# Kernel tuning notes

Hardware: AMD Instinct MI355X
Metric: run time of the kernel (lower is better)

The kernel has to match this reference:

```python
import jax, jax.numpy as jnp
import numpy as np

TAU = 0.05


def setup_inputs() -> dict:
    key = jax.random.key(0)
    ks = jax.random.split(key, 4)
    N, D, F, E = 8192, 1024, 4096, 8
    h = jax.random.normal(ks[0], (N, D), dtype=jnp.float32)
    Wr = jax.random.normal(ks[1], (D, E), dtype=jnp.float32) * (1.0 / np.sqrt(D))
    br = jnp.zeros((E,), dtype=jnp.float32)
    W1 = jax.random.normal(ks[2], (E, D, F), dtype=jnp.float32) * (1.0 / np.sqrt(D))
    b1 = jnp.zeros((E, F), dtype=jnp.float32)
    W2 = jax.random.normal(ks[3], (E, F, D), dtype=jnp.float32) * (1.0 / np.sqrt(F))
    b2 = jnp.zeros((E, D), dtype=jnp.float32)
    return {"h": h, "Wr": Wr, "br": br, "W1": W1, "b1": b1, "W2": W2, "b2": b2}


def reference(h, Wr, br, W1, b1, W2, b2):
    # Router: linear + softmax over experts -> [N, E]
    weights = jax.nn.softmax(h @ Wr + br, axis=-1)
    # Threshold mask (weights > tau); masked_weights = weights * mask
    masked_w = jnp.where(weights > TAU, weights, 0.0)  # [N, E]
    # Experts: 2-layer MLP per expert, computed batched over the expert axis.
    # hid: [N, E, F]
    hid = jax.nn.gelu(jnp.einsum('nd,edf->nef', h, W1) + b1)
    # expert outputs: [N, E, D]
    out_e = jnp.einsum('nef,efd->ned', hid, W2) + b2
    # Weighted combine; zero masked weights annihilate inactive experts,
    # matching the conditional sum (and the zeros_like fallback when none active).
    return jnp.einsum('ne,ned->nd', masked_w, out_e)
```

## Files before the change

### kernel.cpp

```cpp
#include <hip/hip_runtime.h>
#include <hip/hip_bf16.h>
#include <cstdint>
#include <cstddef>

typedef __attribute__((ext_vector_type(8))) __bf16 bf16x8;
typedef __attribute__((ext_vector_type(4))) float f32x4;
typedef __attribute__((ext_vector_type(4))) unsigned short us4;

#define GLOAD_LDS16(g, l)                                                        \
    __builtin_amdgcn_global_load_lds(                                            \
        (const __attribute__((address_space(1))) void*)(g),                      \
        (__attribute__((address_space(3))) void*)(l), 16, 0, 0)

static __device__ __forceinline__ unsigned short f2bf(float x) {
    unsigned int u = __builtin_bit_cast(unsigned int, x);
    return (unsigned short)((u + 0x7FFFu + ((u >> 16) & 1u)) >> 16);
}

static __device__ __forceinline__ float gelu_fast(float x) {
    const float p = x * x;
    const float u = x * fmaf(0.0713548162726f, p, 1.59576912161f);
    const float t = __expf(-u);
    return x * __builtin_amdgcn_rcpf(1.0f + t);
}

__global__ __launch_bounds__(256) void moe_router_kernel(
    const float* __restrict__ h, const float* __restrict__ Wr,
    const float* __restrict__ br, unsigned short* __restrict__ hbf,
    float* __restrict__ mw)
{
    const int lane = threadIdx.x & 63, wave = threadIdx.x >> 6;
    const int n = blockIdx.x * 4 + wave;
    const float* hr = h + (size_t)n * 1024;
    const int base = lane * 16;

    float xs[16];
#pragma unroll
    for (int q = 0; q < 4; ++q) {
        f32x4 v = *(const f32x4*)(hr + base + q * 4);
        xs[q * 4 + 0] = v[0]; xs[q * 4 + 1] = v[1];
        xs[q * 4 + 2] = v[2]; xs[q * 4 + 3] = v[3];
    }
    float acc[8] = {0.f, 0.f, 0.f, 0.f, 0.f, 0.f, 0.f, 0.f};
#pragma unroll
    for (int j = 0; j < 16; ++j) {
        const float x = xs[j];
        const f32x4 w0 = *(const f32x4*)(Wr + (size_t)(base + j) * 8);
        const f32x4 w1 = *(const f32x4*)(Wr + (size_t)(base + j) * 8 + 4);
        acc[0] += x * w0[0]; acc[1] += x * w0[1]; acc[2] += x * w0[2]; acc[3] += x * w0[3];
        acc[4] += x * w1[0]; acc[5] += x * w1[1]; acc[6] += x * w1[2]; acc[7] += x * w1[3];
    }
#pragma unroll
    for (int q = 0; q < 4; ++q) {
        us4 o;
        o[0] = f2bf(xs[q * 4 + 0]); o[1] = f2bf(xs[q * 4 + 1]);
        o[2] = f2bf(xs[q * 4 + 2]); o[3] = f2bf(xs[q * 4 + 3]);
        *(us4*)(hbf + (size_t)n * 1024 + base + q * 4) = o;
    }
#pragma unroll
    for (int m = 32; m >= 1; m >>= 1)
#pragma unroll
        for (int e = 0; e < 8; ++e) acc[e] += __shfl_xor(acc[e], m, 64);

    if (lane == 0) {
        float l[8]; float mx = -1e30f;
#pragma unroll
        for (int e = 0; e < 8; ++e) { l[e] = acc[e] + br[e]; mx = fmaxf(mx, l[e]); }
        float s = 0.f;
#pragma unroll
        for (int e = 0; e < 8; ++e) { l[e] = __expf(l[e] - mx); s += l[e]; }
        const float inv = 1.0f / s;
#pragma unroll
        for (int e = 0; e < 8; ++e) {
            const float w = l[e] * inv;
            mw[(size_t)n * 8 + e] = (w > 0.05f) ? w : 0.0f;
        }
    }
}

__global__ __launch_bounds__(256) void moe_tcvt_kernel(
    const float* __restrict__ in, unsigned short* __restrict__ out,
    int ls, size_t in_es, int os, size_t out_es)
{
    __shared__ unsigned short t[32][33];
    const int e = blockIdx.z;
    const int r = threadIdx.x >> 3, c = (threadIdx.x & 7) * 4;
    const float* I = in + (size_t)e * in_es + (size_t)(blockIdx.x * 32 + r) * ls + blockIdx.y * 32 + c;
    f32x4 v = *(const f32x4*)I;
    t[r][c + 0] = f2bf(v[0]); t[r][c + 1] = f2bf(v[1]);
    t[r][c + 2] = f2bf(v[2]); t[r][c + 3] = f2bf(v[3]);
    __syncthreads();
    unsigned short* O = out + (size_t)e * out_es + (size_t)(blockIdx.y * 32 + r) * os + blockIdx.x * 32 + c;
    us4 o;
    o[0] = t[c + 0][r]; o[1] = t[c + 1][r]; o[2] = t[c + 2][r]; o[3] = t[c + 3][r];
    *(us4*)O = o;
}

#define MFMA_QUAD(MB, NB, AF, BQ)                                              \
  _Pragma("unroll") for (int mi_ = 0; mi_ < 4; ++mi_)                          \
  _Pragma("unroll") for (int ni_ = 0; ni_ < 2; ++ni_) {                        \
      acc[(MB)+mi_][(NB)+ni_] = __builtin_amdgcn_mfma_f32_16x16x32_bf16(       \
          BQ[ni_][1], AF[mi_][1], __builtin_amdgcn_mfma_f32_16x16x32_bf16(     \
          BQ[ni_][0], AF[mi_][0], acc[(MB)+mi_][(NB)+ni_], 0, 0, 0), 0, 0, 0); \
  }

#define BARX()   __builtin_amdgcn_s_barrier()
#define SBX()    __builtin_amdgcn_sched_barrier(0)
#define LGKM(N)  asm volatile("s_waitcnt lgkmcnt(" #N ")" ::: "memory")
#define VMC(N)   asm volatile("s_waitcnt vmcnt(" #N ")" ::: "memory")
#define PRIO1()  __builtin_amdgcn_s_setprio(1)
#define PRIO0()  __builtin_amdgcn_s_setprio(0)

template <int MODE>
__global__ __launch_bounds__(512) void moe_gemm8p(
    const unsigned short* __restrict__ A, int ldga,
    const unsigned short* __restrict__ Bbase, size_t estride, int ldb,
    const float* __restrict__ b1, const float* __restrict__ mw,
    unsigned short* __restrict__ Cg, int ldc,
    float* __restrict__ part,
    int logFc, int f0glob, int kspan, int init)
{
    __shared__ unsigned short sh[65536];
    char* sm = (char*)sh;
    const int XA = 0, XB = 32768, YA = 65536, YB = 98304;

    const int tid = threadIdx.x, lane = tid & 63, wv = tid >> 6;
    const int wr = wv >> 2, wc = wv & 3;

    int bx, by;
    if constexpr (MODE == 0) {
        const int gy = gridDim.y;
        const int orig = blockIdx.x + blockIdx.y * 32;
        const int c8 = orig & 7, j = orig >> 3;
        bx = c8 * 4 + j / gy; by = j % gy;
    } else {
        const int orig = blockIdx.x + blockIdx.y * 32;
        const int c8 = orig & 7, j = orig >> 3;
        bx = c8 * 4 + (j >> 2); by = j & 3;
    }
    const int m0 = bx * 256;
    const int n0 = by * 256;

    const int z = (MODE == 1) ? blockIdx.z : 0;
    const int klo = z * kspan;
    float* Cacc = (MODE == 1) ? part + (size_t)z * (8192 * 1024) : nullptr;

    int e0 = 0, fb = 0;
    const unsigned short* gB0 = nullptr;
    const int rl0 = tid >> 3;
    const int gs8 = ((tid & 7) ^ (rl0 & 7)) * 8;
    if constexpr (MODE == 0) {
        e0 = n0 >> logFc; fb = n0 - (e0 << logFc);
        gB0 = Bbase + (size_t)e0 * estride + (size_t)(fb + rl0) * ldb + gs8;
    }
    const unsigned short* gA0 = A + (size_t)(m0 + rl0) * ldga + gs8;
    const int dstw = wv * 1024;

    auto stageA = [&](int reg, int kk, int q) {
        GLOAD_LDS16(gA0 + kk + (size_t)(q * 64) * ldga,
                    sm + reg + (q >> 1) * 16384 + (q & 1) * 8192 + dstw);
    };
    auto stageB = [&](int reg, int kk, int q) {
        const unsigned short* gb;
        if constexpr (MODE == 0) {
            gb = gB0 + kk;
        } else {
            const int e = kk >> logFc, kc = kk - (e << logFc);
            gb = Bbase + (size_t)e * estride + (size_t)(n0 + rl0) * ldb + kc + gs8;
        }
        GLOAD_LDS16(gb + (size_t)(q * 64) * ldb,
                    sm + reg + (q >> 1) * 16384 + (q & 1) * 8192 + dstw);
    };

    const int l15 = lane & 15, l4 = lane >> 4, l7 = lane & 7;
    const int sA0 = (wr * 128 + l15) * 128 + (((0 + l4) ^ l7) << 4);
    const int sA1 = (wr * 128 + l15) * 128 + (((4 + l4) ^ l7) << 4);
    const int sB0 = (wc * 64 + l15) * 128 + (((0 + l4) ^ l7) << 4);
    const int sB1 = (wc * 64 + l15) * 128 + (((4 + l4) ^ l7) << 4);

    f32x4 acc[8][4] = {};
    bf16x8 afL[4][2], afH[4][2], bqL[2][2], bqH[2][2];

#define RD_AFL(BASE) _Pragma("unroll") for (int mi_=0;mi_<4;++mi_){            \
      afL[mi_][0] = *(const bf16x8*)(sm + (BASE) + sA0 + mi_*2048);            \
      afL[mi_][1] = *(const bf16x8*)(sm + (BASE) + sA1 + mi_*2048); }
#define RD_AFH(BASE) _Pragma("unroll") for (int mi_=0;mi_<4;++mi_){            \
      afH[mi_][0] = *(const bf16x8*)(sm + (BASE) + sA0 + (4+mi_)*2048);        \
      afH[mi_][1] = *(const bf16x8*)(sm + (BASE) + sA1 + (4+mi_)*2048); }
#define RD_BQL(BASE) _Pragma("unroll") for (int ni_=0;ni_<2;++ni_){            \
      bqL[ni_][0] = *(const bf16x8*)(sm + (BASE) + sB0 + ni_*2048);            \
      bqL[ni_][1] = *(const bf16x8*)(sm + (BASE) + sB1 + ni_*2048); }
#define RD_BQH(BASE) _Pragma("unroll") for (int ni_=0;ni_<2;++ni_){            \
      bqH[ni_][0] = *(const bf16x8*)(sm + (BASE) + sB0 + (2+ni_)*2048);        \
      bqH[ni_][1] = *(const bf16x8*)(sm + (BASE) + sB1 + (2+ni_)*2048); }

    const int niter = kspan >> 7;

#pragma unroll
    for (int q = 0; q < 4; ++q) { stageA(XA, klo, q); stageB(XB, klo, q); }
#pragma unroll
    for (int q = 0; q < 4; ++q) { stageA(YA, klo + 64, q); stageB(YB, klo + 64, q); }
    VMC(8); SBX();
    BARX();
    RD_AFL(XA); RD_BQL(XB);

    for (int it = 0; it < niter; ++it) {
        const int kX2 = klo + it * 128 + 128;
        const int kY2 = klo + it * 128 + 192;
        const bool g = (it + 1 < niter);
        RD_BQH(XB);
        BARX(); LGKM(4); SBX(); PRIO1(); MFMA_QUAD(0, 0, afL, bqL); PRIO0(); BARX();
        RD_AFH(XA);
        if (g) { stageA(XA, kX2, 0); stageA(XA, kX2, 2); }
        BARX(); LGKM(8); SBX(); PRIO1(); MFMA_QUAD(0, 2, afL, bqH); PRIO0(); BARX();
        if (g) { stageB(XB, kX2, 0); stageB(XB, kX2, 1); }
        BARX(); LGKM(0); SBX(); PRIO1(); MFMA_QUAD(4, 0, afH, bqL); PRIO0(); BARX();
        if (g) { stageA(XA, kX2, 1); stageA(XA, kX2, 3);
                 stageB(XB, kX2, 2); stageB(XB, kX2, 3);
                 VMC(8); } else { VMC(0); }
        SBX();
        BARX();
        RD_AFL(YA); RD_BQL(YB);
        SBX(); PRIO1(); MFMA_QUAD(4, 2, afH, bqH); PRIO0(); BARX();
        RD_BQH(YB);
        BARX(); LGKM(4); SBX(); PRIO1(); MFMA_QUAD(0, 0, afL, bqL); PRIO0(); BARX();
        RD_AFH(YA);
        if (g) { stageA(YA, kY2, 0); stageA(YA, kY2, 2); }
        BARX(); LGKM(8); SBX(); PRIO1(); MFMA_QUAD(0, 2, afL, bqH); PRIO0(); BARX();
        if (g) { stageB(YB, kY2, 0); stageB(YB, kY2, 1); }
        BARX(); LGKM(0); SBX(); PRIO1(); MFMA_QUAD(4, 0, afH, bqL); PRIO0(); BARX();
        if (g) { stageA(YA, kY2, 1); stageA(YA, kY2, 3);
                 stageB(YB, kY2, 2); stageB(YB, kY2, 3);
                 VMC(8); } else { VMC(0); }
        SBX();
        BARX();
        if (g) { RD_AFL(XA); RD_BQL(XB); }
        SBX(); PRIO1(); MFMA_QUAD(4, 2, afH, bqH); PRIO0(); BARX();
    }

    const int nr0v = l4 * 4;
    if constexpr (MODE == 0) {
        const float* b1p = b1 + (size_t)e0 * 4096 + f0glob + fb;
        f32x4 b1v[4];
#pragma unroll
        for (int j = 0; j < 4; ++j)
            b1v[j] = *(const f32x4*)(b1p + wc * 64 + j * 16 + nr0v);
#pragma unroll
        for (int i = 0; i < 8; ++i) {
            const int token = m0 + wr * 128 + i * 16 + l15;
            const float w = mw[(size_t)token * 8 + e0];
            unsigned short* crow = Cg + (size_t)token * ldc + n0;
#pragma unroll
            for (int j = 0; j < 4; ++j) {
                const int n = wc * 64 + j * 16 + nr0v;
                us4 o;
#pragma unroll
                for (int r = 0; r < 4; ++r)
                    o[r] = f2bf(w * gelu_fast(acc[i][j][r] + b1v[j][r]));
                *(us4*)(crow + n) = o;
            }
        }
    } else {
#pragma unroll
        for (int i = 0; i < 8; ++i) {
            const int row = m0 + wr * 128 + i * 16 + l15;
            float* cp = Cacc + (size_t)row * 1024 + n0;
#pragma unroll
            for (int j = 0; j < 4; ++j) {
                const int n = wc * 64 + j * 16 + nr0v;
                if (init) {
                    *(f32x4*)(cp + n) = acc[i][j];
                } else {
                    f32x4 old = *(const f32x4*)(cp + n);
                    *(f32x4*)(cp + n) = old + acc[i][j];
                }
            }
        }
    }
}

__global__ __launch_bounds__(256) void moe_combine_kernel(
    const float* __restrict__ part, int S,
    float* __restrict__ out, const float* __restrict__ mw,
    const float* __restrict__ b2)
{
    const int n = blockIdx.x, t = threadIdx.x;
    const int d = t * 4;
    f32x4 v = *(const f32x4*)(part + (size_t)n * 1024 + d);
    for (int z = 1; z < S; ++z)
        v = v + *(const f32x4*)(part + (size_t)z * (8192 * 1024) + (size_t)n * 1024 + d);
#pragma unroll
    for (int e = 0; e < 8; ++e) {
        const float w = mw[(size_t)n * 8 + e];
        const f32x4 b = *(const f32x4*)(b2 + (size_t)e * 1024 + d);
        v = v + w * b;
    }
    *(f32x4*)(out + (size_t)n * 1024 + d) = v;
}

extern "C" void kernel_launch(void* const* d_in, const int* in_sizes, int n_in,
                              void* d_out, int out_size, void* d_ws, size_t ws_size,
                              hipStream_t stream)
{
    (void)in_sizes; (void)n_in; (void)out_size;
    const float* h  = (const float*)d_in[0];
    const float* Wr = (const float*)d_in[1];
    const float* br = (const float*)d_in[2];
    const float* W1 = (const float*)d_in[3];
    const float* b1 = (const float*)d_in[4];
    const float* W2 = (const float*)d_in[5];
    const float* b2 = (const float*)d_in[6];
    float* out = (float*)d_out;

    const int N = 8192, D = 1024, F = 4096, E = 8;
    const int S = 2;
    auto al = [](size_t x) { return (x + 255) & ~(size_t)255; };
    const size_t sz_hbf = al((size_t)N * D * 2);
    const size_t sz_mw  = al((size_t)N * E * 4);
    const size_t sz_pt1 = al((size_t)N * D * 4);
    auto tot = [&](int fc) {
        size_t s = sz_hbf + sz_mw + al((size_t)N * ((size_t)E * fc + 32) * 2);
        s += al((size_t)E * fc * D * 2) * 2;
        s += (size_t)S * sz_pt1;
        return s;
    };
    int Fc;
    if      (tot(1024) <= ws_size) Fc = 1024;
    else if (tot(512)  <= ws_size) Fc = 512;
    else                           Fc = 256;
    const int logFc = (Fc == 1024) ? 10 : (Fc == 512) ? 9 : 8;
    const int Kc = E * Fc;
    const int ldAp = Kc + 32;

    char* p = (char*)d_ws;
    unsigned short* hbf = (unsigned short*)p; p += sz_hbf;
    float* mwp  = (float*)p; p += sz_mw;
    unsigned short* ghid = (unsigned short*)p; p += al((size_t)N * (size_t)ldAp * 2);
    unsigned short* W1t  = (unsigned short*)p; p += al((size_t)E * Fc * D * 2);
    unsigned short* W2t  = (unsigned short*)p; p += al((size_t)E * Fc * D * 2);
    float* part = (float*)p;

    moe_router_kernel<<<N / 4, 256, 0, stream>>>(h, Wr, br, hbf, mwp);

    const int nch = F / Fc;
    for (int c = 0; c < nch; ++c) {
        moe_tcvt_kernel<<<dim3(D / 32, Fc / 32, E), 256, 0, stream>>>(
            W1 + (size_t)c * Fc, W1t, F, (size_t)D * F, D, (size_t)Fc * D);
        moe_tcvt_kernel<<<dim3(Fc / 32, D / 32, E), 256, 0, stream>>>(
            W2 + (size_t)c * Fc * D, W2t, D, (size_t)F * D, Fc, (size_t)D * Fc);

        moe_gemm8p<0><<<dim3(32, Kc / 256, 1), 512, 0, stream>>>(
            hbf, 1024, W1t, (size_t)Fc * D, 1024, b1, mwp, ghid, ldAp, nullptr,
            logFc, c * Fc, 1024, 0);

        moe_gemm8p<1><<<dim3(32, 4, S), 512, 0, stream>>>(
            ghid, ldAp, W2t, (size_t)D * Fc, Fc, nullptr, nullptr, nullptr, 0, part,
            logFc, 0, Kc / S, (c == 0) ? 1 : 0);
    }

    moe_combine_kernel<<<N, 256, 0, stream>>>(part, S, out, mwp, b2);
}
```

Measured before the change: 1.266 ms.

## Make first-layer GEMM blocks persistent over four N tiles with continuous K pipeline

Each MODE 0 block now processes four consecutive 256-wide output tiles by running a single pipelined K loop of length 4096 that wraps over the 1024-wide K dimension, emitting the GELU epilogue and resetting accumulators every eight iterations. This removes the pipeline prologue and drain per tile and lets the next tile's loads overlap the current tile's epilogue, and the grid shrinks by four. The trade-off is fewer blocks (less parallelism across CUs), a mid-loop epilogue that adds register pressure and stalls, and a block mapping that assumes the y grid is a multiple of four.

```diff
diff --git a/kernel.cpp b/kernel.cpp
--- a/kernel.cpp
+++ b/kernel.cpp
@@ -129,10 +129,9 @@
 
     int bx, by;
     if constexpr (MODE == 0) {
-        const int gy = gridDim.y;
         const int orig = blockIdx.x + blockIdx.y * 32;
         const int c8 = orig & 7, j = orig >> 3;
-        bx = c8 * 4 + j / gy; by = j % gy;
+        bx = c8 * 4 + (j & 3); by = j >> 2;
     } else {
         const int orig = blockIdx.x + blockIdx.y * 32;
         const int c8 = orig & 7, j = orig >> 3;
@@ -145,26 +144,26 @@
     const int klo = z * kspan;
     float* Cacc = (MODE == 1) ? part + (size_t)z * (8192 * 1024) : nullptr;
 
-    int e0 = 0, fb = 0;
-    const unsigned short* gB0 = nullptr;
     const int rl0 = tid >> 3;
     const int gs8 = ((tid & 7) ^ (rl0 & 7)) * 8;
-    if constexpr (MODE == 0) {
-        e0 = n0 >> logFc; fb = n0 - (e0 << logFc);
-        gB0 = Bbase + (size_t)e0 * estride + (size_t)(fb + rl0) * ldb + gs8;
-    }
     const unsigned short* gA0 = A + (size_t)(m0 + rl0) * ldga + gs8;
     const int dstw = wv * 1024;
 
-    auto stageA = [&](int reg, int kk, int q) {
-        GLOAD_LDS16(gA0 + kk + (size_t)(q * 64) * ldga,
+    auto stageA = [&](int reg, int kv, int q) {
+        const int kcol = (MODE == 0) ? (kv & 1023) : (klo + kv);
+        GLOAD_LDS16(gA0 + kcol + (size_t)(q * 64) * ldga,
                     sm + reg + (q >> 1) * 16384 + (q & 1) * 8192 + dstw);
     };
-    auto stageB = [&](int reg, int kk, int q) {
+    auto stageB = [&](int reg, int kv, int q) {
         const unsigned short* gb;
         if constexpr (MODE == 0) {
-            gb = gB0 + kk;
+            const int tile = kv >> 10;
+            const int n0t = (by * 4 + tile) * 256;
+            const int e = n0t >> logFc, fb = n0t - (e << logFc);
+            gb = Bbase + (size_t)e * estride + (size_t)(fb + rl0) * ldb
+               + (kv & 1023) + gs8;
         } else {
+            const int kk = klo + kv;
             const int e = kk >> logFc, kc = kk - (e << logFc);
             gb = Bbase + (size_t)e * estride + (size_t)(n0 + rl0) * ldb + kc + gs8;
         }
@@ -173,6 +172,7 @@
     };
 
     const int l15 = lane & 15, l4 = lane >> 4, l7 = lane & 7;
+    const int nr0v = l4 * 4;
     const int sA0 = (wr * 128 + l15) * 128 + (((0 + l4) ^ l7) << 4);
     const int sA1 = (wr * 128 + l15) * 128 + (((4 + l4) ^ l7) << 4);
     const int sB0 = (wc * 64 + l15) * 128 + (((0 + l4) ^ l7) << 4);
@@ -197,16 +197,16 @@
     const int niter = kspan >> 7;
 
 #pragma unroll
-    for (int q = 0; q < 4; ++q) { stageA(XA, klo, q); stageB(XB, klo, q); }
-#pragma unroll
-    for (int q = 0; q < 4; ++q) { stageA(YA, klo + 64, q); stageB(YB, klo + 64, q); }
+    for (int q = 0; q < 4; ++q) { stageA(XA, 0, q); stageB(XB, 0, q); }
+#pragma unroll
+    for (int q = 0; q < 4; ++q) { stageA(YA, 64, q); stageB(YB, 64, q); }
     VMC(8); SBX();
     BARX();
     RD_AFL(XA); RD_BQL(XB);
 
     for (int it = 0; it < niter; ++it) {
-        const int kX2 = klo + it * 128 + 128;
-        const int kY2 = klo + it * 128 + 192;
+        const int kX2 = it * 128 + 128;
+        const int kY2 = it * 128 + 192;
         const bool g = (it + 1 < niter);
         RD_BQH(XB);
         BARX(); LGKM(4); SBX(); PRIO1(); MFMA_QUAD(0, 0, afL, bqL); PRIO0(); BARX();
@@ -236,31 +236,35 @@
         BARX();
         if (g) { RD_AFL(XA); RD_BQL(XB); }
         SBX(); PRIO1(); MFMA_QUAD(4, 2, afH, bqH); PRIO0(); BARX();
-    }
-
-    const int nr0v = l4 * 4;
-    if constexpr (MODE == 0) {
-        const float* b1p = b1 + (size_t)e0 * 4096 + f0glob + fb;
-        f32x4 b1v[4];
-#pragma unroll
-        for (int j = 0; j < 4; ++j)
-            b1v[j] = *(const f32x4*)(b1p + wc * 64 + j * 16 + nr0v);
-#pragma unroll
-        for (int i = 0; i < 8; ++i) {
-            const int token = m0 + wr * 128 + i * 16 + l15;
-            const float w = mw[(size_t)token * 8 + e0];
-            unsigned short* crow = Cg + (size_t)token * ldc + n0;
-#pragma unroll
-            for (int j = 0; j < 4; ++j) {
-                const int n = wc * 64 + j * 16 + nr0v;
-                us4 o;
-#pragma unroll
-                for (int r = 0; r < 4; ++r)
-                    o[r] = f2bf(w * gelu_fast(acc[i][j][r] + b1v[j][r]));
-                *(us4*)(crow + n) = o;
+
+        if constexpr (MODE == 0) {
+            if ((it & 7) == 7) {
+                const int tile = it >> 3;
+                const int n0t = (by * 4 + tile) * 256;
+                const int e0t = n0t >> logFc, fbt = n0t - (e0t << logFc);
+                const float* b1p = b1 + (size_t)e0t * 4096 + f0glob + fbt;
+#pragma unroll
+                for (int i = 0; i < 8; ++i) {
+                    const int token = m0 + wr * 128 + i * 16 + l15;
+                    const float w = mw[(size_t)token * 8 + e0t];
+                    unsigned short* crow = Cg + (size_t)token * ldc + n0t;
+#pragma unroll
+                    for (int j = 0; j < 4; ++j) {
+                        const int n = wc * 64 + j * 16 + nr0v;
+                        const f32x4 bv = *(const f32x4*)(b1p + n);
+                        us4 o;
+#pragma unroll
+                        for (int r = 0; r < 4; ++r)
+                            o[r] = f2bf(w * gelu_fast(acc[i][j][r] + bv[r]));
+                        *(us4*)(crow + n) = o;
+                        acc[i][j] = (f32x4){0.f, 0.f, 0.f, 0.f};
+                    }
+                }
             }
         }
-    } else {
+    }
+
+    if constexpr (MODE == 1) {
 #pragma unroll
         for (int i = 0; i < 8; ++i) {
             const int row = m0 + wr * 128 + i * 16 + l15;
@@ -349,9 +353,9 @@
         moe_tcvt_kernel<<<dim3(Fc / 32, D / 32, E), 256, 0, stream>>>(
             W2 + (size_t)c * Fc * D, W2t, D, (size_t)F * D, Fc, (size_t)D * Fc);
 
-        moe_gemm8p<0><<<dim3(32, Kc / 256, 1), 512, 0, stream>>>(
+        moe_gemm8p<0><<<dim3(32, Kc / 1024, 1), 512, 0, stream>>>(
             hbf, 1024, W1t, (size_t)Fc * D, 1024, b1, mwp, ghid, ldAp, nullptr,
-            logFc, c * Fc, 1024, 0);
+            logFc, c * Fc, 4096, 0);
 
         moe_gemm8p<1><<<dim3(32, 4, S), 512, 0, stream>>>(
             ghid, ldAp, W2t, (size_t)D * Fc, Fc, nullptr, nullptr, nullptr, 0, part,
```

Measured after the change: 1.796 ms. +41.9%, slower.
